# Performance work log

Hardware: AMD Instinct MI355X
Metric: run time of the kernel (lower is better)

Reference implementation:

```python
import jax, jax.numpy as jnp
import numpy as np
from itertools import combinations

# 2-source PID on the redundancy lattice (Williams-Beer), antichains indexed
# over sources {0,1}; index 2 is the output variable axis.
FULL = (0, 1, 2)
ANTICHAINS = [((0,), (1,)), ((0,),), ((1,),), ((0, 1),)]  # red, unq0, unq1, syn (cumulative I)
MOEBIUS = np.array([[1, 0, 0, 0],
                    [-1, 1, 0, 0],
                    [-1, 0, 1, 0],
                    [1, -1, -1, 1]], dtype=np.float32)
EPS_DEN = 1e-10
EPS_FRAC = 1e-7


def _marginals(p):
    """Powerset marginals of the joint p over axes (0,1,2); trailing axis = neurons."""
    m = {}
    for r in range(1, 4):
        for a in combinations(FULL, r):
            ax = tuple(sorted(set(FULL) - set(a)))
            m[a] = p.sum(ax, keepdims=True) if ax else p
    return m


def _union(m, alpha):
    """Inclusion-exclusion union probability over the sets in antichain alpha."""
    res = 0.0
    for k in range(1, len(alpha) + 1):
        for beta in combinations(alpha, k):
            b_union = tuple(sorted({b for a in beta for b in a}))
            res = res + ((-1) ** (k - 1)) * m[b_union]
    return res


def _isx(m, alpha, p_full):
    """I_cap^sx for one antichain: sum over joint of p * log2 ratio."""
    p_union = jax.lax.stop_gradient(_union(m, alpha))            # no_grad in original
    alpha_t = tuple(tuple(sorted(a + (2,))) for a in alpha)       # append output var
    p_union_t = _union(m, alpha_t)
    frac = p_union_t / (p_union * m[(2,)] + EPS_DEN)
    frac = jnp.where(frac < EPS_FRAC, jnp.asarray(1.0, frac.dtype), frac)
    return (p_full * jnp.log2(frac)).sum((0, 1, 2))               # -> (N,)


def _pid(p):
    m = _marginals(p)
    I_cap = jnp.stack([_isx(m, a, p) for a in ANTICHAINS])        # (4, N)
    Pi = jnp.asarray(MOEBIUS, p.dtype) @ I_cap                    # Moebius transform (4, N)
    p_out = m[(2,)]                                               # (1, 1, out_bins, N)
    H_tot = -(p_out * jnp.log2(p_out + EPS_DEN)).sum(-2)          # (1, 1, N)
    H_res = (H_tot - I_cap[ANTICHAINS.index(((0, 1),))]).reshape(-1)
    return jnp.concatenate([Pi, H_res[None]], axis=0)             # (5, N): red,unq0,unq1,syn,H_res


def setup_inputs() -> dict:
    key = jax.random.key(0)
    # joint histogram over (src1_bins=16, src2_bins=16, out_bins=2, n_neurons=100000)
    p = jax.random.uniform(key, (16, 16, 2, 100000), dtype=jnp.float32)
    p = p / p.sum((0, 1, 2), keepdims=True)  # normalize to a distribution per neuron
    return {"p_all_neurons": p}


def reference(p_all_neurons):
    return _pid(p_all_neurons)
```

## Files before the change

kernel.cpp:

```cpp
#include <hip/hip_runtime.h>

#define LOG2_EPS_CLAMP -23.2534966f

__device__ __forceinline__ float flog2(float x) { return __builtin_amdgcn_logf(x); }

__global__ __launch_bounds__(256) void pid_kernel(const float* __restrict__ p,
                                                  float* __restrict__ out,
                                                  const int N) {
    __shared__ float lm02[32 * 256];
    const int tid = threadIdx.x;
    const int n = blockIdx.x * 256 + tid;
    if (n >= N) return;
    const float* __restrict__ q = p + n;
    float* __restrict__ c02 = &lm02[tid];

    float m12[32];
    #pragma unroll
    for (int t = 0; t < 32; ++t) m12[t] = 0.f;

    #pragma unroll 1
    for (int i = 0; i < 16; ++i) {
        const float* __restrict__ qi = q + (size_t)(i * 32) * (size_t)N;
        float s0 = 0.f, s1 = 0.f;
        #pragma unroll
        for (int j = 0; j < 16; ++j) {
            const float f0 = qi[(size_t)(2 * j) * (size_t)N];
            const float f1 = qi[(size_t)(2 * j + 1) * (size_t)N];
            s0 += f0; s1 += f1;
            m12[2 * j]     += f0;
            m12[2 * j + 1] += f1;
        }
        c02[(2 * i) * 256]     = s0;
        c02[(2 * i + 1) * 256] = s1;
    }

    float P20 = 0.f, P21 = 0.f;
    #pragma unroll
    for (int j = 0; j < 16; ++j) { P20 += m12[2 * j]; P21 += m12[2 * j + 1]; }
    const float LP20 = flog2(P20);
    const float LP21 = flog2(P21);

    float I1 = 0.f, I2 = 0.f, I4 = 0.f;
    #pragma unroll 1
    for (int i = 0; i < 16; ++i) {
        const float a0  = c02[(2 * i) * 256];
        const float a1  = c02[(2 * i + 1) * 256];
        const float m0i = a0 + a1;
        const float* __restrict__ qi = q + (size_t)(i * 32) * (size_t)N;
        #pragma unroll
        for (int j = 0; j < 16; ++j) {
            const float f0  = qi[(size_t)(2 * j) * (size_t)N];
            const float f1  = qi[(size_t)(2 * j + 1) * (size_t)N];
            const float p01 = f0 + f1;
            const float m1j = m12[2 * j] + m12[2 * j + 1];
            const float u1  = m0i + m1j - p01;
            const float Lu1  = flog2(u1);
            const float Lp01 = flog2(p01);
            {
                const float num = a0 + m12[2 * j] - f0;
                float l1 = flog2(num) - Lu1 - LP20;
                l1 = (l1 < LOG2_EPS_CLAMP) ? 0.f : l1;
                I1 = fmaf(f0, l1, I1);
                float l4 = flog2(f0) - Lp01 - LP20;
                l4 = (l4 < LOG2_EPS_CLAMP) ? 0.f : l4;
                I4 = fmaf(f0, l4, I4);
            }
            {
                const float num = a1 + m12[2 * j + 1] - f1;
                float l1 = flog2(num) - Lu1 - LP21;
                l1 = (l1 < LOG2_EPS_CLAMP) ? 0.f : l1;
                I1 = fmaf(f1, l1, I1);
                float l4 = flog2(f1) - Lp01 - LP21;
                l4 = (l4 < LOG2_EPS_CLAMP) ? 0.f : l4;
                I4 = fmaf(f1, l4, I4);
            }
        }
        {
            const float L0 = flog2(m0i);
            float la = flog2(a0) - L0 - LP20;
            la = (la < LOG2_EPS_CLAMP) ? 0.f : la;
            I2 = fmaf(a0, la, I2);
            float lb = flog2(a1) - L0 - LP21;
            lb = (lb < LOG2_EPS_CLAMP) ? 0.f : lb;
            I2 = fmaf(a1, lb, I2);
        }
    }

    float I3 = 0.f;
    #pragma unroll
    for (int j = 0; j < 16; ++j) {
        const float L1 = flog2(m12[2 * j] + m12[2 * j + 1]);
        float la = flog2(m12[2 * j]) - L1 - LP20;
        la = (la < LOG2_EPS_CLAMP) ? 0.f : la;
        I3 = fmaf(m12[2 * j], la, I3);
        float lb = flog2(m12[2 * j + 1]) - L1 - LP21;
        lb = (lb < LOG2_EPS_CLAMP) ? 0.f : lb;
        I3 = fmaf(m12[2 * j + 1], lb, I3);
    }

    const float H = -(P20 * flog2(P20 + 1e-10f) + P21 * flog2(P21 + 1e-10f));

    out[0 * N + n] = I1;
    out[1 * N + n] = I2 - I1;
    out[2 * N + n] = I3 - I1;
    out[3 * N + n] = I1 - I2 - I3 + I4;
    out[4 * N + n] = H - I4;
}

extern "C" void kernel_launch(void* const* d_in, const int* in_sizes, int n_in,
                              void* d_out, int out_size, void* d_ws, size_t ws_size,
                              hipStream_t stream) {
    const float* p = (const float*)d_in[0];
    float* out = (float*)d_out;
    const int N = in_sizes[0] / 512;
    const int blocks = (N + 255) / 256;
    pid_kernel<<<blocks, 256, 0, stream>>>(p, out, N);
}
```

Baseline: 335.9 us.

## Split each neuron across four lanes with shuffle reductions instead of LDS

Each neuron is now handled by four threads, each owning four of the sixteen source-1 bins. The partial marginals and partial information sums are combined with xor shuffles, which replaces the large shared-memory buffer with registers and launches four times as many blocks. This is meant to raise occupancy and parallelism for a latency-bound, log-heavy kernel. In exchange, adjacent lanes now read addresses that are only 64 neurons apart across a wave, which hurts coalescing, the I3 work is computed redundantly on every lane, and shuffle overhead is added.

```diff
diff --git a/kernel.cpp b/kernel.cpp
--- a/kernel.cpp
+++ b/kernel.cpp
@@ -7,19 +7,21 @@
 __global__ __launch_bounds__(256) void pid_kernel(const float* __restrict__ p,
                                                   float* __restrict__ out,
                                                   const int N) {
-    __shared__ float lm02[32 * 256];
     const int tid = threadIdx.x;
-    const int n = blockIdx.x * 256 + tid;
+    const int g = tid >> 2;
+    const int s = tid & 3;
+    const int n = blockIdx.x * 64 + g;
     if (n >= N) return;
     const float* __restrict__ q = p + n;
-    float* __restrict__ c02 = &lm02[tid];
 
-    float m12[32];
+    float m12p[32];
     #pragma unroll
-    for (int t = 0; t < 32; ++t) m12[t] = 0.f;
+    for (int t = 0; t < 32; ++t) m12p[t] = 0.f;
+    float a0[4], a1[4];
 
-    #pragma unroll 1
-    for (int i = 0; i < 16; ++i) {
+    #pragma unroll
+    for (int ii = 0; ii < 4; ++ii) {
+        const int i = s * 4 + ii;
         const float* __restrict__ qi = q + (size_t)(i * 32) * (size_t)N;
         float s0 = 0.f, s1 = 0.f;
         #pragma unroll
@@ -27,37 +29,42 @@
             const float f0 = qi[(size_t)(2 * j) * (size_t)N];
             const float f1 = qi[(size_t)(2 * j + 1) * (size_t)N];
             s0 += f0; s1 += f1;
-            m12[2 * j]     += f0;
-            m12[2 * j + 1] += f1;
+            m12p[2 * j]     += f0;
+            m12p[2 * j + 1] += f1;
         }
-        c02[(2 * i) * 256]     = s0;
-        c02[(2 * i + 1) * 256] = s1;
+        a0[ii] = s0; a1[ii] = s1;
+    }
+
+    #pragma unroll
+    for (int t = 0; t < 32; ++t) {
+        m12p[t] += __shfl_xor(m12p[t], 1, 64);
+        m12p[t] += __shfl_xor(m12p[t], 2, 64);
     }
 
     float P20 = 0.f, P21 = 0.f;
     #pragma unroll
-    for (int j = 0; j < 16; ++j) { P20 += m12[2 * j]; P21 += m12[2 * j + 1]; }
+    for (int j = 0; j < 16; ++j) { P20 += m12p[2 * j]; P21 += m12p[2 * j + 1]; }
     const float LP20 = flog2(P20);
     const float LP21 = flog2(P21);
 
     float I1 = 0.f, I2 = 0.f, I4 = 0.f;
-    #pragma unroll 1
-    for (int i = 0; i < 16; ++i) {
-        const float a0  = c02[(2 * i) * 256];
-        const float a1  = c02[(2 * i + 1) * 256];
-        const float m0i = a0 + a1;
+    #pragma unroll
+    for (int ii = 0; ii < 4; ++ii) {
+        const int i = s * 4 + ii;
+        const float a0i = a0[ii], a1i = a1[ii];
+        const float m0i = a0i + a1i;
         const float* __restrict__ qi = q + (size_t)(i * 32) * (size_t)N;
         #pragma unroll
         for (int j = 0; j < 16; ++j) {
             const float f0  = qi[(size_t)(2 * j) * (size_t)N];
             const float f1  = qi[(size_t)(2 * j + 1) * (size_t)N];
             const float p01 = f0 + f1;
-            const float m1j = m12[2 * j] + m12[2 * j + 1];
+            const float m1j = m12p[2 * j] + m12p[2 * j + 1];
             const float u1  = m0i + m1j - p01;
             const float Lu1  = flog2(u1);
             const float Lp01 = flog2(p01);
             {
-                const float num = a0 + m12[2 * j] - f0;
+                const float num = a0i + m12p[2 * j] - f0;
                 float l1 = flog2(num) - Lu1 - LP20;
                 l1 = (l1 < LOG2_EPS_CLAMP) ? 0.f : l1;
                 I1 = fmaf(f0, l1, I1);
@@ -66,7 +73,7 @@
                 I4 = fmaf(f0, l4, I4);
             }
             {
-                const float num = a1 + m12[2 * j + 1] - f1;
+                const float num = a1i + m12p[2 * j + 1] - f1;
                 float l1 = flog2(num) - Lu1 - LP21;
                 l1 = (l1 < LOG2_EPS_CLAMP) ? 0.f : l1;
                 I1 = fmaf(f1, l1, I1);
@@ -75,36 +82,40 @@
                 I4 = fmaf(f1, l4, I4);
             }
         }
-        {
-            const float L0 = flog2(m0i);
-            float la = flog2(a0) - L0 - LP20;
-            la = (la < LOG2_EPS_CLAMP) ? 0.f : la;
-            I2 = fmaf(a0, la, I2);
-            float lb = flog2(a1) - L0 - LP21;
-            lb = (lb < LOG2_EPS_CLAMP) ? 0.f : lb;
-            I2 = fmaf(a1, lb, I2);
-        }
+        const float L0 = flog2(m0i);
+        float la = flog2(a0i) - L0 - LP20;
+        la = (la < LOG2_EPS_CLAMP) ? 0.f : la;
+        I2 = fmaf(a0i, la, I2);
+        float lb = flog2(a1i) - L0 - LP21;
+        lb = (lb < LOG2_EPS_CLAMP) ? 0.f : lb;
+        I2 = fmaf(a1i, lb, I2);
     }
+
+    I1 += __shfl_xor(I1, 1, 64); I1 += __shfl_xor(I1, 2, 64);
+    I2 += __shfl_xor(I2, 1, 64); I2 += __shfl_xor(I2, 2, 64);
+    I4 += __shfl_xor(I4, 1, 64); I4 += __shfl_xor(I4, 2, 64);
 
     float I3 = 0.f;
     #pragma unroll
     for (int j = 0; j < 16; ++j) {
-        const float L1 = flog2(m12[2 * j] + m12[2 * j + 1]);
-        float la = flog2(m12[2 * j]) - L1 - LP20;
+        const float L1 = flog2(m12p[2 * j] + m12p[2 * j + 1]);
+        float la = flog2(m12p[2 * j]) - L1 - LP20;
         la = (la < LOG2_EPS_CLAMP) ? 0.f : la;
-        I3 = fmaf(m12[2 * j], la, I3);
-        float lb = flog2(m12[2 * j + 1]) - L1 - LP21;
+        I3 = fmaf(m12p[2 * j], la, I3);
+        float lb = flog2(m12p[2 * j + 1]) - L1 - LP21;
         lb = (lb < LOG2_EPS_CLAMP) ? 0.f : lb;
-        I3 = fmaf(m12[2 * j + 1], lb, I3);
+        I3 = fmaf(m12p[2 * j + 1], lb, I3);
     }
 
     const float H = -(P20 * flog2(P20 + 1e-10f) + P21 * flog2(P21 + 1e-10f));
 
-    out[0 * N + n] = I1;
-    out[1 * N + n] = I2 - I1;
-    out[2 * N + n] = I3 - I1;
-    out[3 * N + n] = I1 - I2 - I3 + I4;
-    out[4 * N + n] = H - I4;
+    if (s == 0) {
+        out[0 * N + n] = I1;
+        out[1 * N + n] = I2 - I1;
+        out[2 * N + n] = I3 - I1;
+        out[3 * N + n] = I1 - I2 - I3 + I4;
+        out[4 * N + n] = H - I4;
+    }
 }
 
 extern "C" void kernel_launch(void* const* d_in, const int* in_sizes, int n_in,
@@ -113,6 +124,6 @@
     const float* p = (const float*)d_in[0];
     float* out = (float*)d_out;
     const int N = in_sizes[0] / 512;
-    const int blocks = (N + 255) / 256;
+    const int blocks = (N + 63) / 64;
     pid_kernel<<<blocks, 256, 0, stream>>>(p, out, N);
 }
```

New measurement: 285.5 us. -15.0%, faster.
